# Kernel optimization log

Hardware: AMD Instinct MI355X
Metric: run time of the kernel (lower is better)

The kernel has to match this reference:

```python
import jax, jax.numpy as jnp
import numpy as np

B, N, D, A = 256, 32, 128, 16
DOA, E, FD, H, O = 144, 128, 128, 256, 1  # obs_act_in, obs_out/embed, final_in, hidden, final_out


def setup_inputs() -> dict:
    key = jax.random.key(0)
    ks = jax.random.split(key, 12)
    p = lambda k, shape: jax.random.normal(k, shape, jnp.float32) * 0.05
    return {
        "states": jax.random.normal(ks[0], (B, N, D), jnp.float32),
        "policies": jax.random.uniform(ks[1], (B, N, A), dtype=jnp.float32),
        "actions": jax.random.uniform(ks[2], (B, N, A), dtype=jnp.float32),
        "Wk_proc": p(ks[3], (D, E)),
        "Wq_proc": p(ks[4], (D, E)),
        "Wv_proc": p(ks[5], (D, E)),
        "Wk": p(ks[6], (E, FD)),
        "Wq": p(ks[7], (E, FD)),
        "We": p(ks[8], (DOA, E)),
        "Wav": p(ks[9], (E, FD)),
        "W1": p(ks[10], (FD, H)),
        "W2": p(ks[11], (H, O)),
    }


def reference(states, policies, actions, Wk_proc, Wq_proc, Wv_proc, Wk, Wq, We, Wav, W1, W2):
    n = states.shape[1]
    # NOTE: original code divides BOTH attention stages by sqrt(self.d_k_obs) = final_input_dim
    scale = 1.0 / jnp.sqrt(jnp.asarray(Wk.shape[1], states.dtype))

    # stage-1 attention over agents [B,N,N]
    k1 = states @ Wk_proc
    q1 = states @ Wq_proc
    v1 = states @ Wv_proc
    w1 = jax.nn.softmax(jnp.einsum('bie,bje->bij', q1, k1) * scale, axis=-1)
    wav1 = jnp.einsum('bij,bje->bie', w1, v1)  # [B,N,E]

    # stage-2 attention weights
    k2 = wav1 @ Wk
    q2 = wav1 @ Wq
    w2 = jax.nn.softmax(jnp.einsum('bif,bjf->bij', q2, k2) * scale, axis=-1)

    # build obs-action/policy tensor: entry [b,i,j] uses policy of agent j when i==j else action of j
    oa = jnp.concatenate([states, actions], axis=-1)   # [B,N,DOA]
    op = jnp.concatenate([states, policies], axis=-1)  # [B,N,DOA]
    eye = jnp.eye(n, dtype=states.dtype)[:, :, None]   # [N,N,1]
    oap = eye * op[:, None, :, :] + (1.0 - eye) * oa[:, None, :, :]  # [B,N,N,DOA]

    av = (oap @ We) @ Wav  # [B,N,N,FD]

    # node_features[b,i,j,f] = sum_k w2[b,i,k] * av[b,j,k,f]  (avoids the 5D repeat)
    node = jnp.einsum('bik,bjkf->bijf', w2, av)

    h = node @ W1
    h = jnp.where(h > 0, h, 0.01 * h)  # leaky_relu, default slope
    value = h @ W2  # [B,N,N,O]
    return value, w1, w2
```

## Files before the change

kernel.cpp:

```cpp
#include <hip/hip_runtime.h>
#include <math.h>

#define NB 256
#define NN 32
#define DD 128
#define NA 16
#define HH 256

using f32x4v  = __attribute__((ext_vector_type(4))) float;
using bf16x8  = __attribute__((ext_vector_type(8))) short;

static __device__ __forceinline__ float4 ld4(const float* p){ return *reinterpret_cast<const float4*>(p); }
static __device__ __forceinline__ void st4f(float* p, float4 v){ *reinterpret_cast<float4*>(p) = v; }
static __device__ __forceinline__ float elem(float4 v, int kk){
    return (kk==0)?v.x:(kk==1)?v.y:(kk==2)?v.z:v.w;
}

static __device__ __forceinline__ unsigned f2bf(float x){
    unsigned u = __float_as_uint(x);
    u += 0x7fffu + ((u >> 16) & 1u);
    return u >> 16;
}
static __device__ __forceinline__ unsigned pack2(float a, float b){
    return f2bf(a) | (f2bf(b) << 16);
}
static __device__ __forceinline__ float bf2f(unsigned short s){
    return __uint_as_float(((unsigned)s) << 16);
}

static __device__ __forceinline__ f32x4v mfma16(bf16x8 a, bf16x8 b, f32x4v c){
    return __builtin_amdgcn_mfma_f32_16x16x32_bf16(a, b, c, 0, 0, 0);
}

static __device__ __forceinline__ void store_frag(unsigned short* __restrict__ dst,
                                                  int frag, int l, const float v[8]){
    uint4 p;
    p.x = pack2(v[0], v[1]); p.y = pack2(v[2], v[3]);
    p.z = pack2(v[4], v[5]); p.w = pack2(v[6], v[7]);
    *reinterpret_cast<uint4*>(dst + (size_t)(frag*64 + l)*8) = p;
}

__global__ __launch_bounds__(1024)
void k_pre(const float* __restrict__ We, const float* __restrict__ Wav,
           const float* __restrict__ W1,
           const float* __restrict__ Wqp, const float* __restrict__ Wkp,
           const float* __restrict__ Wvp, const float* __restrict__ Wq,
           const float* __restrict__ Wk,
           float* __restrict__ WABf, unsigned short* __restrict__ WABs,
           unsigned short* __restrict__ Wqps, unsigned short* __restrict__ Wkps,
           unsigned short* __restrict__ Wvps, unsigned short* __restrict__ Wqs,
           unsigned short* __restrict__ Wks)
{
    __shared__ float W1c[128*16];
    __shared__ float WABt[160*16];
    const int t = threadIdx.x;
    const int bid = blockIdx.x;

    if (bid < 16) {
        const int ct = bid;

        {
            int k = t >> 3, c2 = (t & 7) * 2;
            *reinterpret_cast<float2*>(W1c + k*16 + c2) =
                *reinterpret_cast<const float2*>(W1 + k*256 + ct*16 + c2);
        }
        __syncthreads();

        const int m = t >> 3, cq2 = (t & 7) * 2;
        float a1x = 0.f, a1y = 0.f;
        {
            const float* wrow = Wav + m*128;
            #pragma unroll 4
            for (int k0 = 0; k0 < 128; k0 += 4) {
                float4 xv = ld4(wrow + k0);
                #pragma unroll
                for (int kk = 0; kk < 4; kk++) {
                    float2 wr = *reinterpret_cast<const float2*>(W1c + (k0+kk)*16 + cq2);
                    float x = elem(xv, kk);
                    a1x = fmaf(x, wr.x, a1x);
                    a1y = fmaf(x, wr.y, a1y);
                }
            }
        }
        __syncthreads();
        W1c[m*16 + cq2]     = a1x;
        W1c[m*16 + cq2 + 1] = a1y;
        __syncthreads();

        const int rg = t >> 4, c = t & 15;
        float a20 = 0.f, a21 = 0.f, a22 = 0.f;
        {
            #pragma unroll 2
            for (int k0 = 0; k0 < 128; k0 += 4) {
                float4 xv0 = ld4(We + rg*128 + k0);
                float4 xv1 = ld4(We + (rg+64)*128 + k0);
                float4 xv2 = (rg < 16) ? ld4(We + (128+rg)*128 + k0)
                                       : make_float4(0.f,0.f,0.f,0.f);
                #pragma unroll
                for (int kk = 0; kk < 4; kk++) {
                    float w = W1c[(k0+kk)*16 + c];
                    a20 = fmaf(elem(xv0,kk), w, a20);
                    a21 = fmaf(elem(xv1,kk), w, a21);
                    a22 = fmaf(elem(xv2,kk), w, a22);
                }
            }
        }
        WABt[rg*16 + c]      = a20;
        WABt[(rg+64)*16 + c] = a21;
        if (rg < 32) WABt[(128+rg)*16 + c] = a22;
        if (rg < 16) WABf[(size_t)(128 + rg)*256 + ct*16 + c] = a22;
        __syncthreads();

        if (t < 320) {
            int kt = t >> 6, l = t & 63;
            float v[8];
            #pragma unroll
            for (int i = 0; i < 8; i++)
                v[i] = WABt[(kt*32 + (l>>4)*8 + i)*16 + (l&15)];
            store_frag(WABs, kt*16 + ct, l, v);
        }
    } else {
        const int sel = (bid - 16) >> 1, half = (bid - 16) & 1;
        const float* W = (sel==0) ? Wqp : (sel==1) ? Wkp : (sel==2) ? Wvp :
                         (sel==3) ? Wq : Wk;
        unsigned short* dst = (sel==0) ? Wqps : (sel==1) ? Wkps : (sel==2) ? Wvps :
                              (sel==3) ? Wqs : Wks;
        int s = half*1024 + t;
        int frag = s >> 6, l = s & 63;
        int kt = frag >> 3, nt = frag & 7;
        float v[8];
        #pragma unroll
        for (int i=0;i<8;i++)
            v[i] = W[(kt*32 + (l>>4)*8 + i)*128 + nt*16 + (l&15)];
        store_frag(dst, frag, l, v);
    }
}

static __device__ __forceinline__ void scores_softmax512(const float* __restrict__ Qm,
                                                         const float* __restrict__ Km,
                                                         float scale,
                                                         float* __restrict__ w_lds,
                                                         float* __restrict__ w_out,
                                                         int i, int j)
{
    float s0 = 0.f, s1 = 0.f;
    #pragma unroll 4
    for (int k=0;k<128;k+=4){
        float4 qv = ld4(Qm + i*132 + k);
        float4 k0 = ld4(Km + j*132 + k);
        float4 k1 = ld4(Km + (j+16)*132 + k);
        s0 += qv.x*k0.x + qv.y*k0.y + qv.z*k0.z + qv.w*k0.w;
        s1 += qv.x*k1.x + qv.y*k1.y + qv.z*k1.z + qv.w*k1.w;
    }
    s0 *= scale; s1 *= scale;
    float m = fmaxf(s0, s1);
    #pragma unroll
    for (int d=1; d<16; d<<=1) m = fmaxf(m, __shfl_xor(m, d));
    float e0 = expf(s0 - m), e1 = expf(s1 - m);
    float sum = e0 + e1;
    #pragma unroll
    for (int d=1; d<16; d<<=1) sum += __shfl_xor(sum, d);
    float inv = 1.f / sum;
    e0 *= inv; e1 *= inv;
    w_lds[i*36 + j]      = e0;
    w_lds[i*36 + j + 16] = e1;
    w_out[i*32 + j]      = e0;
    w_out[i*32 + j + 16] = e1;
}

__global__ __launch_bounds__(512)
void k_main(const float* __restrict__ states, const float* __restrict__ pol,
            const float* __restrict__ act,
            const unsigned short* __restrict__ Wqps, const unsigned short* __restrict__ Wkps,
            const unsigned short* __restrict__ Wvps, const unsigned short* __restrict__ Wqs,
            const unsigned short* __restrict__ Wks,  const unsigned short* __restrict__ WABs,
            const float* __restrict__ WABf, const float* __restrict__ W2,
            float* __restrict__ out_v, float* __restrict__ out_w1,
            float* __restrict__ out_w2)
{
    const int b = blockIdx.x;
    const int t = threadIdx.x;
    const float scale = 0.08838834764831845f;

    __shared__ float SH[16000];
    float* B1   = SH;
    float* B2   = SH + 4224;
    float* Wb2f = SH + 8448;
    float* Wb1f = SH + 9600;
    float* APd  = SH + 10752;
    unsigned short* Xoa  = (unsigned short*)(SH + 11264);
    unsigned short* Ubf  = (unsigned short*)B1;
    unsigned short* Wvbf = (unsigned short*)B2;
    float*    A1 = SH;
    unsigned* P2 = (unsigned*)(SH + 11904);
    unsigned* Q2 = (unsigned*)SH;
    float* SPQ = Wb1f;

    const float* stg  = states + (size_t)b*(NN*DD);
    const float* actg = act + (size_t)b*(NN*NA);
    const float* polg = pol + (size_t)b*(NN*NA);

    {
        int r = t >> 4, kb = t & 15;
        #pragma unroll
        for (int uu = 0; uu < 10; uu++){
            int k = kb + 16*uu;
            float v = (k < 128) ? stg[r*128 + k]
                    : (k < 144) ? actg[r*16 + (k-128)] : 0.f;
            Xoa[r*168 + k] = (unsigned short)f2bf(v);
        }
        if (t < 128) {
            int rr = t>>2, cc = (t&3)*4;
            float4 p = ld4(polg + rr*16 + cc), a = ld4(actg + rr*16 + cc);
            st4f(APd + rr*16 + cc, make_float4(p.x-a.x, p.y-a.y, p.z-a.z, p.w-a.w));
        }
    }
    __syncthreads();

    const int l    = t & 63;
    const int wv   = t >> 6;
    const int mt   = wv & 1;
    const int ntb  = (wv >> 1) * 2;
    const int nb7  = (wv >> 1) * 4;
    const int arow = mt*16 + (l & 15);
    const int drow = mt*16 + ((l >> 4) << 2);
    const int dcol = l & 15;

    const int c  = t & 127;
    const int g  = t >> 7;
    const int cp = (t & 127)*2;
    const int si = t >> 4;
    const int sj = t & 15;
    const int wp = wv & 1;

    float qr0[8], qr1[8], sq[8];
    {
        #pragma unroll
        for (int u=0;u<8;u++){ qr0[u]=0.f; qr1[u]=0.f; }
        const float* wB = WABf + 128*256;
        #pragma unroll
        for (int k0=0;k0<16;k0+=4){
            float4 xv[8];
            #pragma unroll
            for (int u=0;u<8;u++) xv[u] = ld4(APd + (g*8+u)*16 + k0);
            #pragma unroll
            for (int kk=0;kk<4;kk++){
                float2 w = *reinterpret_cast<const float2*>(wB + (k0+kk)*256 + cp);
                #pragma unroll
                for (int u=0;u<8;u++){
                    float x = elem(xv[u],kk);
                    qr0[u] = fmaf(x, w.x, qr0[u]);
                    qr1[u] = fmaf(x, w.y, qr1[u]);
                }
            }
        }
        float2 w2v = *reinterpret_cast<const float2*>(W2 + cp);
        #pragma unroll
        for (int u=0;u<8;u++) sq[u] = qr0[u]*w2v.x + qr1[u]*w2v.y;
        #pragma unroll
        for (int d=1; d<64; d<<=1){
            #pragma unroll
            for (int u=0;u<8;u++) sq[u] += __shfl_xor(sq[u], d);
        }
    }

    {
        f32x4v aq0={0.f,0.f,0.f,0.f}, aq1={0.f,0.f,0.f,0.f};
        f32x4v ak0={0.f,0.f,0.f,0.f}, ak1={0.f,0.f,0.f,0.f};
        const unsigned short* ab = Xoa + arow*168 + (l>>4)*8;
        #pragma unroll
        for (int kt = 0; kt < 4; kt++){
            bf16x8 a   = *reinterpret_cast<const bf16x8*>(ab + kt*32);
            bf16x8 bq0 = *reinterpret_cast<const bf16x8*>(Wqps + (size_t)((kt*8+ntb  )*64 + l)*8);
            bf16x8 bq1 = *reinterpret_cast<const bf16x8*>(Wqps + (size_t)((kt*8+ntb+1)*64 + l)*8);
            bf16x8 bk0 = *reinterpret_cast<const bf16x8*>(Wkps + (size_t)((kt*8+ntb  )*64 + l)*8);
            bf16x8 bk1 = *reinterpret_cast<const bf16x8*>(Wkps + (size_t)((kt*8+ntb+1)*64 + l)*8);
            aq0 = mfma16(a, bq0, aq0); aq1 = mfma16(a, bq1, aq1);
            ak0 = mfma16(a, bk0, ak0); ak1 = mfma16(a, bk1, ak1);
        }
        #pragma unroll
        for (int r = 0; r < 4; r++){
            B1[(drow+r)*132 + ntb*16     + dcol] = aq0[r];
            B1[(drow+r)*132 + (ntb+1)*16 + dcol] = aq1[r];
            B2[(drow+r)*132 + ntb*16     + dcol] = ak0[r];
            B2[(drow+r)*132 + (ntb+1)*16 + dcol] = ak1[r];
        }
    }

    f32x4v ac[4];
    {
        #pragma unroll
        for (int n=0;n<4;n++) ac[n] = f32x4v{0.f,0.f,0.f,0.f};
        const unsigned short* ab = Xoa + arow*168 + (l>>4)*8;
        #pragma unroll
        for (int kt = 0; kt < 5; kt++){
            bf16x8 a = *reinterpret_cast<const bf16x8*>(ab + kt*32);
            #pragma unroll
            for (int n = 0; n < 4; n++){
                bf16x8 bb = *reinterpret_cast<const bf16x8*>(WABs + (size_t)((kt*16 + nb7 + n)*64 + l)*8);
                ac[n] = mfma16(a, bb, ac[n]);
            }
        }
    }
    __syncthreads();

    scores_softmax512(B1, B2, scale, Wb1f, out_w1 + (size_t)b*1024, si, sj);
    __syncthreads();

    {
        float au[8];
        #pragma unroll
        for (int u=0;u<8;u++) au[u]=0.f;
        #pragma unroll
        for (int k0=0;k0<32;k0+=4){
            float4 xv[8];
            #pragma unroll
            for (int u=0;u<8;u++) xv[u] = ld4(Wb1f + (g*8+u)*36 + k0);
            #pragma unroll
            for (int kk=0;kk<4;kk++){
                float w = bf2f(Xoa[(k0+kk)*168 + c]);
                #pragma unroll
                for (int u=0;u<8;u++) au[u] = fmaf(elem(xv[u],kk), w, au[u]);
            }
        }
        #pragma unroll
        for (int u=0;u<8;u++) Ubf[(g*8+u)*136 + c] = (unsigned short)f2bf(au[u]);
    }
    __syncthreads();

    {
        f32x4v av0={0.f,0.f,0.f,0.f}, av1={0.f,0.f,0.f,0.f};
        const unsigned short* ab = Ubf + arow*136 + (l>>4)*8;
        #pragma unroll
        for (int kt = 0; kt < 4; kt++){
            bf16x8 a  = *reinterpret_cast<const bf16x8*>(ab + kt*32);
            bf16x8 b0 = *reinterpret_cast<const bf16x8*>(Wvps + (size_t)((kt*8+ntb  )*64 + l)*8);
            bf16x8 b1 = *reinterpret_cast<const bf16x8*>(Wvps + (size_t)((kt*8+ntb+1)*64 + l)*8);
            av0 = mfma16(a, b0, av0); av1 = mfma16(a, b1, av1);
        }
        #pragma unroll
        for (int r = 0; r < 4; r++){
            Wvbf[(drow+r)*136 + ntb*16     + dcol] = (unsigned short)f2bf(av0[r]);
            Wvbf[(drow+r)*136 + (ntb+1)*16 + dcol] = (unsigned short)f2bf(av1[r]);
        }
    }
    __syncthreads();

    {
        f32x4v aq0={0.f,0.f,0.f,0.f}, aq1={0.f,0.f,0.f,0.f};
        f32x4v ak0={0.f,0.f,0.f,0.f}, ak1={0.f,0.f,0.f,0.f};
        const unsigned short* ab = Wvbf + arow*136 + (l>>4)*8;
        #pragma unroll
        for (int kt = 0; kt < 4; kt++){
            bf16x8 a   = *reinterpret_cast<const bf16x8*>(ab + kt*32);
            bf16x8 bq0 = *reinterpret_cast<const bf16x8*>(Wqs + (size_t)((kt*8+ntb  )*64 + l)*8);
            bf16x8 bq1 = *reinterpret_cast<const bf16x8*>(Wqs + (size_t)((kt*8+ntb+1)*64 + l)*8);
            bf16x8 bk0 = *reinterpret_cast<const bf16x8*>(Wks + (size_t)((kt*8+ntb  )*64 + l)*8);
            bf16x8 bk1 = *reinterpret_cast<const bf16x8*>(Wks + (size_t)((kt*8+ntb+1)*64 + l)*8);
            aq0 = mfma16(a, bq0, aq0); aq1 = mfma16(a, bq1, aq1);
            ak0 = mfma16(a, bk0, ak0); ak1 = mfma16(a, bk1, ak1);
        }
        __syncthreads();
        #pragma unroll
        for (int r = 0; r < 4; r++){
            B1[(drow+r)*132 + ntb*16     + dcol] = aq0[r];
            B1[(drow+r)*132 + (ntb+1)*16 + dcol] = aq1[r];
            B2[(drow+r)*132 + ntb*16     + dcol] = ak0[r];
            B2[(drow+r)*132 + (ntb+1)*16 + dcol] = ak1[r];
        }
    }
    __syncthreads();

    scores_softmax512(B1, B2, scale, Wb2f, out_w2 + (size_t)b*1024, si, sj);
    __syncthreads();

    {
        #pragma unroll
        for (int n = 0; n < 4; n++){
            #pragma unroll
            for (int r = 0; r < 4; r++)
                A1[(drow+r)*260 + (nb7+n)*16 + dcol] = ac[n][r];
        }
    }
    __syncthreads();

    {
        float ap0[8], ap1[8];
        #pragma unroll
        for (int u=0;u<8;u++){ ap0[u]=0.f; ap1[u]=0.f; }
        #pragma unroll
        for (int k0=0;k0<32;k0+=4){
            float4 xv[8];
            #pragma unroll
            for (int u=0;u<8;u++) xv[u] = ld4(Wb2f + (g*8+u)*36 + k0);
            #pragma unroll
            for (int kk=0;kk<4;kk++){
                float2 w = *reinterpret_cast<const float2*>(A1 + (k0+kk)*260 + cp);
                #pragma unroll
                for (int u=0;u<8;u++){
                    float x = elem(xv[u],kk);
                    ap0[u] = fmaf(x, w.x, ap0[u]);
                    ap1[u] = fmaf(x, w.y, ap1[u]);
                }
            }
        }
        #pragma unroll
        for (int u=0;u<8;u++)
            P2[(g*8+u)*128 + (cp>>1)] = pack2(ap0[u], ap1[u]);
        float2 w2v = *reinterpret_cast<const float2*>(W2 + cp);
        float sp[8];
        #pragma unroll
        for (int u=0;u<8;u++) sp[u] = ap0[u]*w2v.x + ap1[u]*w2v.y;
        #pragma unroll
        for (int d=1; d<64; d<<=1){
            #pragma unroll
            for (int u=0;u<8;u++) sp[u] += __shfl_xor(sp[u], d);
        }
        if (l == 0){
            #pragma unroll
            for (int u=0;u<8;u++) SPQ[(g*8+u)*2 + wp] = sp[u];
        }
    }
    __syncthreads();

    {
        #pragma unroll
        for (int u=0;u<8;u++)
            Q2[(g*8+u)*132 + (cp>>1)] = pack2(qr0[u], qr1[u]);
        if (l == 0){
            #pragma unroll
            for (int u=0;u<8;u++) SPQ[64 + (g*8+u)*2 + wp] = sq[u];
        }
    }
    __syncthreads();

    {
        float w00 = Wb2f[si*36 + sj], w01 = Wb2f[si*36 + sj + 16];
        float SPi = SPQ[si*2] + SPQ[si*2+1];
        float SQa = SPQ[64 + sj*2] + SPQ[64 + sj*2+1];
        float SQb = SPQ[64 + (sj+16)*2] + SPQ[64 + (sj+16)*2+1];
        float a0 = 0.f, a1 = 0.f;

        #define PROC(PA,QA,QB,H2) {                                         \
            float w2e = W2[(H2)], w2o = W2[(H2)+1];                         \
            float paE = __uint_as_float((PA)<<16), paO = __uint_as_float((PA) & 0xffff0000u); \
            float qaE = __uint_as_float((QA)<<16), qaO = __uint_as_float((QA) & 0xffff0000u); \
            float qbE = __uint_as_float((QB)<<16), qbO = __uint_as_float((QB) & 0xffff0000u); \
            float t0 = fmaf(w00, qaE, paE); a0 = fmaf(fabsf(t0), w2e, a0);  \
            float t1 = fmaf(w00, qaO, paO); a0 = fmaf(fabsf(t1), w2o, a0);  \
            float t2 = fmaf(w01, qbE, paE); a1 = fmaf(fabsf(t2), w2e, a1);  \
            float t3 = fmaf(w01, qbO, paO); a1 = fmaf(fabsf(t3), w2o, a1); }

        #pragma unroll 4
        for (int hp4 = 0; hp4 < 32; hp4++){
            uint4 pa4 = *reinterpret_cast<const uint4*>(P2 + si*128 + hp4*4);
            uint4 qa4 = *reinterpret_cast<const uint4*>(Q2 + sj*132 + hp4*4);
            uint4 qb4 = *reinterpret_cast<const uint4*>(Q2 + (sj+16)*132 + hp4*4);
            PROC(pa4.x, qa4.x, qb4.x, hp4*8+0)
            PROC(pa4.y, qa4.y, qb4.y, hp4*8+2)
            PROC(pa4.z, qa4.z, qb4.z, hp4*8+4)
            PROC(pa4.w, qa4.w, qb4.w, hp4*8+6)
        }
        #undef PROC

        float* ov = out_v + (size_t)b*1024;
        ov[si*32 + sj]      = fmaf(0.495f, a0, 0.505f*(SPi + w00*SQa));
        ov[si*32 + sj + 16] = fmaf(0.495f, a1, 0.505f*(SPi + w01*SQb));
    }
}

extern "C" void kernel_launch(void* const* d_in, const int* in_sizes, int n_in,
                              void* d_out, int out_size, void* d_ws, size_t ws_size,
                              hipStream_t stream) {
    const float* states = (const float*)d_in[0];
    const float* pol    = (const float*)d_in[1];
    const float* act    = (const float*)d_in[2];
    const float* Wkp    = (const float*)d_in[3];
    const float* Wqp    = (const float*)d_in[4];
    const float* Wvp    = (const float*)d_in[5];
    const float* Wk     = (const float*)d_in[6];
    const float* Wq     = (const float*)d_in[7];
    const float* We     = (const float*)d_in[8];
    const float* Wav    = (const float*)d_in[9];
    const float* W1     = (const float*)d_in[10];
    const float* W2     = (const float*)d_in[11];

    float* out    = (float*)d_out;
    float* out_v  = out;
    float* out_w1 = out + 256*1024;
    float* out_w2 = out + 2*256*1024;

    float* WABf = (float*)d_ws;
    unsigned short* WABs = (unsigned short*)(WABf + 36864);
    unsigned short* wsu  = (unsigned short*)(WABf + 57344);
    unsigned short* Wqps = wsu;
    unsigned short* Wkps = wsu + 16384;
    unsigned short* Wvps = wsu + 32768;
    unsigned short* Wqs  = wsu + 49152;
    unsigned short* Wks  = wsu + 65536;

    hipLaunchKernelGGL(k_pre, dim3(26), dim3(1024), 0, stream,
                       We, Wav, W1, Wqp, Wkp, Wvp, Wq, Wk,
                       WABf, WABs, Wqps, Wkps, Wvps, Wqs, Wks);
    hipLaunchKernelGGL(k_main, dim3(NB), dim3(512), 0, stream,
                       states, pol, act,
                       Wqps, Wkps, Wvps, Wqs, Wks, WABs, WABf, W2,
                       out_v, out_w1, out_w2);
}
```

Baseline: 44.97 us.

## Split weight-precompute kernel into two stages with wider parallelism

The single 26-block weight-preprocessing kernel is replaced by two kernels. The first computes Wav@W1 across 32 blocks, staging chunks of W1 in shared memory, and converts the five projection weights to bf16 fragments in parallel blocks. The second, 16 blocks, multiplies We by that intermediate using We tiles staged in shared memory. The goal is to spread the serial preprocessing chain over more CUs and use coalesced tile loads. The cost is an extra kernel launch and a global round-trip for the intermediate.

```diff
diff --git a/kernel.cpp b/kernel.cpp
--- a/kernel.cpp
+++ b/kernel.cpp
@@ -40,99 +40,128 @@
     *reinterpret_cast<uint4*>(dst + (size_t)(frag*64 + l)*8) = p;
 }
 
-__global__ __launch_bounds__(1024)
-void k_pre(const float* __restrict__ We, const float* __restrict__ Wav,
-           const float* __restrict__ W1,
-           const float* __restrict__ Wqp, const float* __restrict__ Wkp,
-           const float* __restrict__ Wvp, const float* __restrict__ Wq,
-           const float* __restrict__ Wk,
-           float* __restrict__ WABf, unsigned short* __restrict__ WABs,
-           unsigned short* __restrict__ Wqps, unsigned short* __restrict__ Wkps,
-           unsigned short* __restrict__ Wvps, unsigned short* __restrict__ Wqs,
-           unsigned short* __restrict__ Wks)
+__global__ __launch_bounds__(512)
+void k_pre0(const float* __restrict__ Wav, const float* __restrict__ W1,
+            const float* __restrict__ Wqp, const float* __restrict__ Wkp,
+            const float* __restrict__ Wvp, const float* __restrict__ Wq,
+            const float* __restrict__ Wk,
+            float* __restrict__ T2g,
+            unsigned short* __restrict__ Wqps, unsigned short* __restrict__ Wkps,
+            unsigned short* __restrict__ Wvps, unsigned short* __restrict__ Wqs,
+            unsigned short* __restrict__ Wks)
 {
-    __shared__ float W1c[128*16];
-    __shared__ float WABt[160*16];
     const int t = threadIdx.x;
     const int bid = blockIdx.x;
 
-    if (bid < 16) {
-        const int ct = bid;
-
-        {
-            int k = t >> 3, c2 = (t & 7) * 2;
-            *reinterpret_cast<float2*>(W1c + k*16 + c2) =
-                *reinterpret_cast<const float2*>(W1 + k*256 + ct*16 + c2);
-        }
-        __syncthreads();
-
-        const int m = t >> 3, cq2 = (t & 7) * 2;
-        float a1x = 0.f, a1y = 0.f;
-        {
-            const float* wrow = Wav + m*128;
-            #pragma unroll 4
-            for (int k0 = 0; k0 < 128; k0 += 4) {
-                float4 xv = ld4(wrow + k0);
-                #pragma unroll
-                for (int kk = 0; kk < 4; kk++) {
-                    float2 wr = *reinterpret_cast<const float2*>(W1c + (k0+kk)*16 + cq2);
-                    float x = elem(xv, kk);
-                    a1x = fmaf(x, wr.x, a1x);
-                    a1y = fmaf(x, wr.y, a1y);
-                }
-            }
-        }
-        __syncthreads();
-        W1c[m*16 + cq2]     = a1x;
-        W1c[m*16 + cq2 + 1] = a1y;
-        __syncthreads();
-
-        const int rg = t >> 4, c = t & 15;
-        float a20 = 0.f, a21 = 0.f, a22 = 0.f;
-        {
-            #pragma unroll 2
-            for (int k0 = 0; k0 < 128; k0 += 4) {
-                float4 xv0 = ld4(We + rg*128 + k0);
-                float4 xv1 = ld4(We + (rg+64)*128 + k0);
-                float4 xv2 = (rg < 16) ? ld4(We + (128+rg)*128 + k0)
-                                       : make_float4(0.f,0.f,0.f,0.f);
-                #pragma unroll
-                for (int kk = 0; kk < 4; kk++) {
-                    float w = W1c[(k0+kk)*16 + c];
-                    a20 = fmaf(elem(xv0,kk), w, a20);
-                    a21 = fmaf(elem(xv1,kk), w, a21);
-                    a22 = fmaf(elem(xv2,kk), w, a22);
-                }
-            }
-        }
-        WABt[rg*16 + c]      = a20;
-        WABt[(rg+64)*16 + c] = a21;
-        if (rg < 32) WABt[(128+rg)*16 + c] = a22;
-        if (rg < 16) WABf[(size_t)(128 + rg)*256 + ct*16 + c] = a22;
-        __syncthreads();
-
-        if (t < 320) {
-            int kt = t >> 6, l = t & 63;
-            float v[8];
-            #pragma unroll
-            for (int i = 0; i < 8; i++)
-                v[i] = WABt[(kt*32 + (l>>4)*8 + i)*16 + (l&15)];
-            store_frag(WABs, kt*16 + ct, l, v);
-        }
+    if (bid < 32) {
+        __shared__ float WavR[4*128];
+        __shared__ float W1c[16*256];
+        if (t < 128) st4f(WavR + t*4, ld4(Wav + (size_t)bid*4*128 + t*4));
+
+        const int c  = t & 255;
+        const int rp = (t >> 8) * 2;
+        float acc0 = 0.f, acc1 = 0.f;
+
+        for (int ch = 0; ch < 8; ch++) {
+            __syncthreads();
+            #pragma unroll
+            for (int u = 0; u < 2; u++) {
+                int idx = t + 512*u;
+                int row = idx >> 6, c4 = (idx & 63) * 4;
+                st4f(W1c + row*256 + c4, ld4(W1 + (size_t)(ch*16 + row)*256 + c4));
+            }
+            __syncthreads();
+            #pragma unroll
+            for (int kk = 0; kk < 16; kk++) {
+                float w  = W1c[kk*256 + c];
+                acc0 = fmaf(WavR[rp*128     + ch*16 + kk], w, acc0);
+                acc1 = fmaf(WavR[(rp+1)*128 + ch*16 + kk], w, acc1);
+            }
+        }
+        T2g[(size_t)(bid*4 + rp)*256 + c]     = acc0;
+        T2g[(size_t)(bid*4 + rp + 1)*256 + c] = acc1;
     } else {
-        const int sel = (bid - 16) >> 1, half = (bid - 16) & 1;
+        const int bb = bid - 32;
+        const int fg = bb*8 + (t >> 6);
+        const int l  = t & 63;
+        const int sel = fg >> 5, frag = fg & 31;
+        const int kt = frag >> 3, nt = frag & 7;
         const float* W = (sel==0) ? Wqp : (sel==1) ? Wkp : (sel==2) ? Wvp :
                          (sel==3) ? Wq : Wk;
         unsigned short* dst = (sel==0) ? Wqps : (sel==1) ? Wkps : (sel==2) ? Wvps :
                               (sel==3) ? Wqs : Wks;
-        int s = half*1024 + t;
-        int frag = s >> 6, l = s & 63;
-        int kt = frag >> 3, nt = frag & 7;
         float v[8];
         #pragma unroll
-        for (int i=0;i<8;i++)
+        for (int i = 0; i < 8; i++)
             v[i] = W[(kt*32 + (l>>4)*8 + i)*128 + nt*16 + (l&15)];
         store_frag(dst, frag, l, v);
+    }
+}
+
+__global__ __launch_bounds__(512)
+void k_pre1(const float* __restrict__ We, const float* __restrict__ T2g,
+            float* __restrict__ WABf, unsigned short* __restrict__ WABs)
+{
+    __shared__ float T2c[16*132];
+    __shared__ float WeC[48*128];
+    __shared__ float WABt[160*16];
+
+    const int t = threadIdx.x;
+    const int ct = blockIdx.x;
+
+    {
+        int row = t >> 2, c4 = (t & 3) * 4;
+        float4 v = ld4(T2g + (size_t)row*256 + ct*16 + c4);
+        T2c[(c4+0)*132 + row] = v.x;
+        T2c[(c4+1)*132 + row] = v.y;
+        T2c[(c4+2)*132 + row] = v.z;
+        T2c[(c4+3)*132 + row] = v.w;
+    }
+    if (t < 256) WABt[(144 + (t>>4))*16 + (t&15)] = 0.f;
+
+    const int rg = t >> 4;
+    const int c  = t & 15;
+
+    for (int c3 = 0; c3 < 3; c3++) {
+        const int rows48 = c3 * 48;
+        __syncthreads();
+        #pragma unroll
+        for (int u = 0; u < 3; u++) {
+            int idx = t + 512*u;
+            int row = idx >> 5, c4 = (idx & 31) * 4;
+            st4f(WeC + row*128 + c4, ld4(We + (size_t)(rows48 + row)*128 + c4));
+        }
+        __syncthreads();
+
+        float accA = 0.f, accB = 0.f;
+        #pragma unroll 4
+        for (int k0 = 0; k0 < 128; k0 += 4) {
+            float4 wa = ld4(WeC + rg*128 + k0);
+            float4 wb = ld4(WeC + (rg+32)*128 + k0);
+            float4 tv = ld4(T2c + c*132 + k0);
+            #pragma unroll
+            for (int kk = 0; kk < 4; kk++) {
+                float tvk = elem(tv, kk);
+                accA = fmaf(elem(wa,kk), tvk, accA);
+                accB = fmaf(elem(wb,kk), tvk, accB);
+            }
+        }
+        WABt[(rows48 + rg)*16 + c] = accA;
+        if (rg < 16) {
+            WABt[(rows48 + rg + 32)*16 + c] = accB;
+            if (c3 == 2)
+                WABf[(size_t)(128 + rg)*256 + ct*16 + c] = accB;
+        }
+    }
+    __syncthreads();
+
+    if (t < 320) {
+        int kt = t >> 6, l = t & 63;
+        float v[8];
+        #pragma unroll
+        for (int i = 0; i < 8; i++)
+            v[i] = WABt[(kt*32 + (l>>4)*8 + i)*16 + (l&15)];
+        store_frag(WABs, kt*16 + ct, l, v);
     }
 }
 
@@ -498,10 +527,13 @@
     unsigned short* Wvps = wsu + 32768;
     unsigned short* Wqs  = wsu + 49152;
     unsigned short* Wks  = wsu + 65536;
-
-    hipLaunchKernelGGL(k_pre, dim3(26), dim3(1024), 0, stream,
-                       We, Wav, W1, Wqp, Wkp, Wvp, Wq, Wk,
-                       WABf, WABs, Wqps, Wkps, Wvps, Wqs, Wks);
+    float* T2g = WABf + 98304;
+
+    hipLaunchKernelGGL(k_pre0, dim3(52), dim3(512), 0, stream,
+                       Wav, W1, Wqp, Wkp, Wvp, Wq, Wk,
+                       T2g, Wqps, Wkps, Wvps, Wqs, Wks);
+    hipLaunchKernelGGL(k_pre1, dim3(16), dim3(512), 0, stream,
+                       We, T2g, WABf, WABs);
     hipLaunchKernelGGL(k_main, dim3(NB), dim3(512), 0, stream,
                        states, pol, act,
                        Wqps, Wkps, Wvps, Wqs, Wks, WABs, WABf, W2,
```

New measurement: 45.84 us. Within noise of the previous version (+1.9%).
